# Kernel optimization log

Hardware: AMD Instinct MI355X
Metric: run time of the kernel (lower is better)

The kernel has to match this reference:

```python
import jax, jax.numpy as jnp
import numpy as np

K = 20
NEG_SLOPE = 0.2
BN_EPS = 1e-5


def knn_idx(x, k):
    # x: (B, C, N) -> neighbor indices (B, N, k) by largest negative sq-distance
    xt = jnp.swapaxes(x, 1, 2)                      # (B, N, C)
    inner = 2.0 * jnp.einsum('bic,bjc->bij', xt, xt)
    sq = jnp.sum(xt * xt, axis=-1)                  # (B, N)
    dist = inner - sq[:, :, None] - sq[:, None, :]  # -||xi-xj||^2
    _, idx = jax.lax.top_k(dist, k)
    return idx


def edge_feature(x, src, idx):
    # x: (B, C, N) centers; src: (B, C, M) gather source; idx: (B, N, k)
    xt = jnp.swapaxes(x, 1, 2)                      # (B, N, C)
    st = jnp.swapaxes(src, 1, 2)                    # (B, M, C)
    b = jnp.arange(xt.shape[0])[:, None, None]
    neigh = st[b, idx]                              # (B, N, k, C)
    center = xt[:, :, None, :]                      # (B, N, 1, C)
    feat = jnp.concatenate(
        [neigh - center, jnp.broadcast_to(center, neigh.shape)], axis=-1)
    return jnp.transpose(feat, (0, 3, 1, 2))        # (B, 2C, N, k)


def conv_bn_lrelu(x, w, gamma, beta):
    # 1x1 conv (no bias) + training-mode BatchNorm2d + LeakyReLU(0.2)
    y = jnp.einsum('oc,bcnk->bonk', w, x)
    mean = jnp.mean(y, axis=(0, 2, 3), keepdims=True)
    var = jnp.var(y, axis=(0, 2, 3), keepdims=True)
    y = (y - mean) * jax.lax.rsqrt(var + BN_EPS)
    y = y * gamma[None, :, None, None] + beta[None, :, None, None]
    return jnp.where(y >= 0, y, NEG_SLOPE * y)


def knn_ia_idx(x, y, k):
    # cosine-similarity KNN from x (B,Cx,N) into y (B,Cy,M), normalize over channels
    xn = x / jnp.maximum(jnp.linalg.norm(x, axis=1, keepdims=True), 1e-12)
    yn = y / jnp.maximum(jnp.linalg.norm(y, axis=1, keepdims=True), 1e-12)
    simi = jnp.einsum('bci,bcj->bij', xn, yn)       # (B, N, M)
    _, idx = jax.lax.top_k(simi, k)
    return idx


def setup_inputs() -> dict:
    key = jax.random.key(0)
    ks = jax.random.split(key, 8)
    B, N, M, EMB = 8, 1024, 1024, 512
    x = jax.random.normal(ks[0], (B, 3, N), dtype=jnp.float32)
    y = jax.random.normal(ks[1], (B, 128, M), dtype=jnp.float32)
    def w(k_, o, c):
        return jax.random.normal(k_, (o, c), dtype=jnp.float32) * (1.0 / np.sqrt(c))
    inp = {
        'x': x, 'y': y,
        'w1': w(ks[2], 64, 6),
        'w2': w(ks[3], 64, 128),
        'w3': w(ks[4], 128, 128),
        'w4': w(ks[5], 256, 256),
        'w5': w(ks[6], EMB, 512),
        'g1': jnp.ones(64), 'b1': jnp.zeros(64),
        'g2': jnp.ones(64), 'b2': jnp.zeros(64),
        'g3': jnp.ones(128), 'b3': jnp.zeros(128),
        'g4': jnp.ones(256), 'b4': jnp.zeros(256),
        'g5': jnp.ones(EMB), 'b5': jnp.zeros(EMB),
    }
    return inp


def reference(x, y, w1, w2, w3, w4, w5, g1, b1, g2, b2, g3, b3, g4, b4, g5, b5):
    # block 1
    h = conv_bn_lrelu(edge_feature(x, x, knn_idx(x, K)), w1, g1, b1)
    x1 = jnp.max(h, axis=-1)                        # (B, 64, N)
    # block 2
    h = conv_bn_lrelu(edge_feature(x1, x1, knn_idx(x1, K)), w2, g2, b2)
    x2 = jnp.max(h, axis=-1)                        # (B, 64, N)
    # block 3
    h = conv_bn_lrelu(edge_feature(x2, x2, knn_idx(x2, K)), w3, g3, b3)
    x3 = jnp.max(h, axis=-1)                        # (B, 128, N)
    # block 4: cross-attention KNN into y (cosine similarity)
    h = conv_bn_lrelu(edge_feature(x3, y, knn_ia_idx(x3, y, K)), w4, g4, b4)
    x4 = jnp.max(h, axis=-1)                        # (B, 256, N)
    # final 1x1 conv + BN + LeakyReLU on concatenated features (512 ch)
    cat = jnp.concatenate([x1, x2, x3, x4], axis=1)  # (B, 512, N)
    out = conv_bn_lrelu(cat[..., None], w5, g5, b5)[..., 0]
    return out                                       # (B, n_emb_dims, N)
```

## Files before the change

kernel.cpp:

```cpp
#include <hip/hip_runtime.h>
#include <hip/hip_bf16.h>

#define KNN 20
#define NEG_SLOPE 0.2f

constexpr int BB = 8;
constexpr int NN = 1024;
constexpr int MM = 1024;

typedef short bf16x8 __attribute__((ext_vector_type(8)));
typedef float f32x4 __attribute__((ext_vector_type(4)));
typedef double f64x4 __attribute__((ext_vector_type(4)));
typedef unsigned long long u64;

__device__ __forceinline__ u64 pack_key64(double d, int j) {
  u64 u = (u64)__double_as_longlong(d);
  u = (u & 0x8000000000000000ULL) ? ~u : (u | 0x8000000000000000ULL);
  return (u & ~(u64)1023) | (u64)(1023 - j);
}

__device__ __forceinline__ void topk20_u64(u64 (&s)[16], int lane, int* op) {
#pragma unroll
  for (int p = 1; p < 16; p <<= 1) {
#pragma unroll
    for (int k = p; k >= 1; k >>= 1) {
#pragma unroll
      for (int j = k % p; j + k < 16; j += 2 * k) {
#pragma unroll
        for (int i = 0; i < k; ++i) {
          int a = j + i, b = j + i + k;
          if (b < 16 && (a / (2 * p)) == (b / (2 * p))) {
            u64 hi = s[a] > s[b] ? s[a] : s[b];
            u64 lo = s[a] > s[b] ? s[b] : s[a];
            s[a] = hi;
            s[b] = lo;
          }
        }
      }
    }
  }
#pragma unroll
  for (int r = 0; r < KNN; ++r) {
    u64 win = s[0];
#pragma unroll
    for (int off = 32; off > 0; off >>= 1) {
      u64 o = __shfl_xor(win, off, 64);
      win = o > win ? o : win;
    }
    if (lane == 0) op[r] = 1023 - (int)(win & (u64)1023);
    if (s[0] == win) {
#pragma unroll
      for (int i = 0; i < 15; ++i) s[i] = s[i + 1];
      s[15] = 0ULL;
    }
  }
}

__global__ void k_probe_mfma(int* __restrict__ rowt, int* __restrict__ colt,
                             int* __restrict__ flag) {
  __shared__ int cnt[256];
  __shared__ int oksh;
  int tid = threadIdx.x;
  if (tid == 0) oksh = 1;
  for (int e = tid; e < 256; e += 64) cnt[e] = 0;
  __syncthreads();
  int lane = tid & 63;
  f64x4 z = {0.0, 0.0, 0.0, 0.0};
  double ai = (double)(lane & 15);
  double p3 = 1.0, p5 = 1.0;
  int kq = lane >> 4;
  for (int t = 0; t < kq; ++t) { p3 *= 3.0; p5 *= 5.0; }
  f64x4 d1 = __builtin_amdgcn_mfma_f64_16x16x4f64(ai, 1.0, z, 0, 0, 0);
  f64x4 d2 = __builtin_amdgcn_mfma_f64_16x16x4f64(1.0, ai, z, 0, 0, 0);
  f64x4 d3 = __builtin_amdgcn_mfma_f64_16x16x4f64(p3, p5, z, 0, 0, 0);
  bool ok = true;
  int ri[4], ci[4];
#pragma unroll
  for (int r = 0; r < 4; ++r) {
    double va = d1[r], vb = d2[r], vp = d3[r];
    int i = (int)(va * 0.25);
    int j = (int)(vb * 0.25);
    bool e_ok = (i >= 0) && (i < 16) && (j >= 0) && (j < 16) &&
                (va == 4.0 * (double)i) && (vb == 4.0 * (double)j) && (vp == 3616.0);
    if (e_ok) {
      atomicAdd(&cnt[i * 16 + j], 1);
    } else {
      ok = false;
      i = 0;
      j = 0;
    }
    ri[r] = i;
    ci[r] = j;
  }
  if (!ok) atomicExch(&oksh, 0);
  __syncthreads();
  bool bij = true;
  for (int e = tid; e < 256; e += 64)
    if (cnt[e] != 1) bij = false;
  if (!bij) atomicExch(&oksh, 0);
  __syncthreads();
#pragma unroll
  for (int r = 0; r < 4; ++r) {
    rowt[lane * 4 + r] = ri[r];
    colt[lane * 4 + r] = ci[r];
  }
  if (tid == 0) *flag = oksh;
}

__global__ __launch_bounds__(256) void k_transpose_d(
    const float* __restrict__ in, double* __restrict__ out, int C, int Np) {
  int total = BB * C * Np;
  for (int t = blockIdx.x * 256 + threadIdx.x; t < total; t += gridDim.x * 256) {
    int c = t % C;
    int n = (t / C) % Np;
    int b = t / (C * Np);
    out[t] = (double)in[((size_t)b * C + c) * Np + n];
  }
}

__global__ __launch_bounds__(256) void k_cvt_bf16(
    const float* __restrict__ in, __hip_bfloat16* __restrict__ out, int n) {
  int i = blockIdx.x * 256 + threadIdx.x;
  if (i < n) out[i] = __float2bfloat16(in[i]);
}

template <int RECIP>
__global__ __launch_bounds__(256) void k_rowsq(
    const double* __restrict__ A, int ld, int C, double* __restrict__ sq) {
  int p = blockIdx.x * 256 + threadIdx.x;
  if (p >= BB * NN) return;
  const double* row = A + (size_t)p * ld;
  double s = 0.0;
  for (int c = 0; c < C; ++c) { double v = row[c]; s += v * v; }
  if (RECIP) {
    sq[p] = 1.0 / fmax(sqrt(s), 1e-12);
  } else {
    sq[p] = s;
  }
}

__global__ __launch_bounds__(256) void k_knn3(
    const double* __restrict__ xs3, const double* __restrict__ sq, int* __restrict__ idx) {
  __shared__ double P[NN * 3];
  int b = blockIdx.x;
  const double* Xb = xs3 + (size_t)b * NN * 3;
  int tid = threadIdx.x;
  for (int t = tid; t < NN * 3; t += 256) P[t] = Xb[t];
  __syncthreads();
  int wave = tid >> 6, lane = tid & 63;
  int i = blockIdx.y * 4 + wave;
  double xi = P[i * 3], yi = P[i * 3 + 1], zi = P[i * 3 + 2];
  double sqi = sq[b * NN + i];
  u64 s[16];
#pragma unroll
  for (int m = 0; m < 16; ++m) {
    int j = m * 64 + lane;
    double d = fma(xi, P[j * 3], 0.0);
    d = fma(yi, P[j * 3 + 1], d);
    d = fma(zi, P[j * 3 + 2], d);
    s[m] = pack_key64(2.0 * d - sqi - sq[b * NN + j], j);
  }
  int* op = idx + ((size_t)b * NN + i) * KNN;
  topk20_u64(s, lane, op);
}

template <int MODE>
__global__ __launch_bounds__(256) void k_gram_u(
    const double* __restrict__ A, int lda, const double* __restrict__ Bm, int ldb,
    const double* __restrict__ sqA, const double* __restrict__ sqB,
    u64* __restrict__ kk, int C, int b0, const int* __restrict__ rowt,
    const int* __restrict__ colt, const int* __restrict__ flag) {
  __shared__ double As[2][16][132];
  __shared__ double Bs[2][16][68];
  int bg = b0 + blockIdx.x;
  int bl = blockIdx.x;
  int j0 = blockIdx.y * 64;
  int i0 = blockIdx.z * 128;
  const double* Ab = A + (size_t)bg * NN * lda;
  const double* Bb = Bm + (size_t)bg * MM * ldb;
  int tid = threadIdx.x;
  if (*flag) {
    int lane = tid & 63, w = tid >> 6;
    int lm = lane & 15, lq = lane >> 4;
    f64x4 acc[2][4] = {};
    for (int r = 0; r < 8; ++r) {
      int li = tid + r * 256;
      int row = li >> 4, k = li & 15;
      As[0][k][row] = Ab[(size_t)(i0 + row) * lda + k];
    }
    for (int r = 0; r < 4; ++r) {
      int li = tid + r * 256;
      int row = li >> 4, k = li & 15;
      Bs[0][k][row] = Bb[(size_t)(j0 + row) * ldb + k];
    }
    __syncthreads();
    int nblk = C >> 4;
    for (int cb = 0; cb < nblk; ++cb) {
      int buf = cb & 1;
      double ra[8], rb[4];
      bool pf = (cb + 1 < nblk);
      if (pf) {
        int c0 = (cb + 1) << 4;
        for (int r = 0; r < 8; ++r) {
          int li = tid + r * 256;
          int row = li >> 4, k = li & 15;
          ra[r] = Ab[(size_t)(i0 + row) * lda + c0 + k];
        }
        for (int r = 0; r < 4; ++r) {
          int li = tid + r * 256;
          int row = li >> 4, k = li & 15;
          rb[r] = Bb[(size_t)(j0 + row) * ldb + c0 + k];
        }
      }
#pragma unroll
      for (int kc = 0; kc < 4; ++kc) {
        double a0 = As[buf][kc * 4 + lq][w * 16 + lm];
        double a1 = As[buf][kc * 4 + lq][64 + w * 16 + lm];
#pragma unroll
        for (int t = 0; t < 4; ++t) {
          double b = Bs[buf][kc * 4 + lq][t * 16 + lm];
          acc[0][t] = __builtin_amdgcn_mfma_f64_16x16x4f64(a0, b, acc[0][t], 0, 0, 0);
          acc[1][t] = __builtin_amdgcn_mfma_f64_16x16x4f64(a1, b, acc[1][t], 0, 0, 0);
        }
      }
      if (pf) {
        int nb = buf ^ 1;
        for (int r = 0; r < 8; ++r) {
          int li = tid + r * 256;
          int row = li >> 4, k = li & 15;
          As[nb][k][row] = ra[r];
        }
        for (int r = 0; r < 4; ++r) {
          int li = tid + r * 256;
          int row = li >> 4, k = li & 15;
          Bs[nb][k][row] = rb[r];
        }
      }
      __syncthreads();
    }
    int rta[4], cta[4];
#pragma unroll
    for (int r = 0; r < 4; ++r) {
      rta[r] = rowt[lane * 4 + r];
      cta[r] = colt[lane * 4 + r];
    }
#pragma unroll
    for (int g = 0; g < 2; ++g) {
#pragma unroll
      for (int t = 0; t < 4; ++t) {
#pragma unroll
        for (int r = 0; r < 4; ++r) {
          int i = i0 + g * 64 + w * 16 + rta[r];
          int j = j0 + t * 16 + cta[r];
          double v = acc[g][t][r];
          if (MODE == 1)
            v = 2.0 * v - sqA[(size_t)bg * NN + i] - sqB[(size_t)bg * MM + j];
          if (MODE == 2) v = v * sqA[(size_t)bg * NN + i] * sqB[(size_t)bg * MM + j];
          kk[((size_t)bl * NN + i) * MM + j] = pack_key64(v, j);
        }
      }
    }
  } else {
    int tx = tid & 15, ty = tid >> 4;
    double acc[8][4] = {};
    for (int c0 = 0; c0 < C; c0 += 16) {
      if (c0) __syncthreads();
      for (int r = 0; r < 8; ++r) {
        int li = tid + r * 256;
        int row = li >> 4, k = li & 15;
        As[0][k][row] = Ab[(size_t)(i0 + row) * lda + c0 + k];
      }
      for (int r = 0; r < 4; ++r) {
        int li = tid + r * 256;
        int row = li >> 4, k = li & 15;
        Bs[0][k][row] = Bb[(size_t)(j0 + row) * ldb + c0 + k];
      }
      __syncthreads();
#pragma unroll
      for (int k = 0; k < 16; ++k) {
        double a_[8], b_[4];
#pragma unroll
        for (int ii = 0; ii < 8; ++ii) a_[ii] = As[0][k][ty * 8 + ii];
#pragma unroll
        for (int jj = 0; jj < 4; ++jj) b_[jj] = Bs[0][k][jj * 16 + tx];
#pragma unroll
        for (int ii = 0; ii < 8; ++ii)
#pragma unroll
          for (int jj = 0; jj < 4; ++jj)
            acc[ii][jj] = fma(a_[ii], b_[jj], acc[ii][jj]);
      }
    }
    for (int ii = 0; ii < 8; ++ii) {
      int i = i0 + ty * 8 + ii;
      double qa = sqA[(size_t)bg * NN + i];
      for (int jj = 0; jj < 4; ++jj) {
        int j = j0 + jj * 16 + tx;
        double v = acc[ii][jj];
        if (MODE == 1) v = 2.0 * v - qa - sqB[(size_t)bg * MM + j];
        if (MODE == 2) v = v * qa * sqB[(size_t)bg * MM + j];
        kk[((size_t)bl * NN + i) * MM + j] = pack_key64(v, j);
      }
    }
  }
}

__global__ __launch_bounds__(256) void k_topk(const u64* __restrict__ kk,
                                              int* __restrict__ idx, int b0) {
  int wave = threadIdx.x >> 6;
  int lane = threadIdx.x & 63;
  int bl = blockIdx.x;
  int row = blockIdx.y * 4 + wave;
  const u64* rp = kk + ((size_t)bl * NN + row) * MM;
  u64 s[16];
#pragma unroll
  for (int m = 0; m < 16; ++m) s[m] = rp[m * 64 + lane];
  int* op = idx + ((size_t)(b0 + bl) * NN + row) * KNN;
  topk20_u64(s, lane, op);
}

__global__ __launch_bounds__(256) void k_featmm2(
    const double* __restrict__ src0, int ld0, int Np0,
    const double* __restrict__ src1, int ld1,
    const float* __restrict__ w, int CW,
    double* __restrict__ out0, double* __restrict__ out1, int C, int O,
    const int* __restrict__ rowt, const int* __restrict__ colt,
    const int* __restrict__ flag) {
  __shared__ double As[16][68];
  __shared__ double Ws[16][68];
  int nbo = O >> 6;
  int b = blockIdx.x;
  int mode = blockIdx.y >= nbo;
  int o0 = (blockIdx.y - (mode ? nbo : 0)) * 64;
  int j0 = blockIdx.z * 64;
  const double* src = mode ? src1 : src0;
  int lds_ = mode ? ld1 : ld0;
  int Np = mode ? NN : Np0;
  double* out = mode ? out1 : out0;
  int tid = threadIdx.x;
  const double* Sb = src + (size_t)b * Np * lds_;
  if (*flag) {
    int lane = tid & 63, wv = tid >> 6;
    int lm = lane & 15, lq = lane >> 4;
    f64x4 acc[4] = {};
    for (int c0 = 0; c0 < C; c0 += 16) {
      if (c0) __syncthreads();
      for (int r = 0; r < 4; ++r) {
        int li = tid + r * 256;
        int row = li >> 4, k = li & 15;
        int c = c0 + k;
        As[k][row] = (c < C) ? Sb[(size_t)(j0 + row) * lds_ + c] : 0.0;
        double wvv = 0.0;
        if (c < C) {
          const float* wr = w + (size_t)(o0 + row) * CW;
          wvv = (mode == 0) ? (double)wr[c] : ((double)wr[C + c] - (double)wr[c]);
        }
        Ws[k][row] = wvv;
      }
      __syncthreads();
#pragma unroll
      for (int kc = 0; kc < 4; ++kc) {
        double a = As[kc * 4 + lq][wv * 16 + lm];
#pragma unroll
        for (int t = 0; t < 4; ++t) {
          double bb = Ws[kc * 4 + lq][t * 16 + lm];
          acc[t] = __builtin_amdgcn_mfma_f64_16x16x4f64(a, bb, acc[t], 0, 0, 0);
        }
      }
    }
    int rta[4], cta[4];
#pragma unroll
    for (int r = 0; r < 4; ++r) {
      rta[r] = rowt[lane * 4 + r];
      cta[r] = colt[lane * 4 + r];
    }
#pragma unroll
    for (int t = 0; t < 4; ++t) {
#pragma unroll
      for (int r = 0; r < 4; ++r) {
        int j = j0 + wv * 16 + rta[r];
        int o = o0 + t * 16 + cta[r];
        out[((size_t)b * Np + j) * O + o] = acc[t][r];
      }
    }
  } else {
    int tx = tid & 15, ty = tid >> 4;
    double acc[4][4] = {};
    for (int c0 = 0; c0 < C; c0 += 16) {
      if (c0) __syncthreads();
      for (int r = 0; r < 4; ++r) {
        int li = tid + r * 256;
        int row = li >> 4, k = li & 15;
        int c = c0 + k;
        As[k][row] = (c < C) ? Sb[(size_t)(j0 + row) * lds_ + c] : 0.0;
        double wvv = 0.0;
        if (c < C) {
          const float* wr = w + (size_t)(o0 + row) * CW;
          wvv = (mode == 0) ? (double)wr[c] : ((double)wr[C + c] - (double)wr[c]);
        }
        Ws[k][row] = wvv;
      }
      __syncthreads();
#pragma unroll
      for (int k = 0; k < 16; ++k) {
        double a_[4], b_[4];
#pragma unroll
        for (int ii = 0; ii < 4; ++ii) a_[ii] = As[k][ty * 4 + ii];
#pragma unroll
        for (int jj = 0; jj < 4; ++jj) b_[jj] = Ws[k][tx * 4 + jj];
#pragma unroll
        for (int ii = 0; ii < 4; ++ii)
#pragma unroll
          for (int jj = 0; jj < 4; ++jj)
            acc[ii][jj] = fma(a_[ii], b_[jj], acc[ii][jj]);
      }
    }
    for (int ii = 0; ii < 4; ++ii) {
      int j = j0 + ty * 4 + ii;
      double* op = &out[((size_t)b * Np + j) * O + o0 + tx * 4];
      double2 v0, v1;
      v0.x = acc[ii][0];
      v0.y = acc[ii][1];
      v1.x = acc[ii][2];
      v1.y = acc[ii][3];
      *(double2*)op = v0;
      *(double2*)(op + 2) = v1;
    }
  }
}

__global__ __launch_bounds__(256) void k_gemm5_mfma(
    const __hip_bfloat16* __restrict__ cath, const __hip_bfloat16* __restrict__ w5h,
    float* __restrict__ out) {
  int b = blockIdx.x;
  int j0 = blockIdx.y * 16;
  int o0 = blockIdx.z * 64 + (threadIdx.x >> 6) * 16;
  int lane = threadIdx.x & 63;
  int m = lane & 15;
  int quad = lane >> 4;
  const __hip_bfloat16* arow = cath + ((size_t)b * NN + j0 + m) * 512 + quad * 8;
  const __hip_bfloat16* brow = w5h + (size_t)(o0 + m) * 512 + quad * 8;
  f32x4 acc = {0.f, 0.f, 0.f, 0.f};
#pragma unroll
  for (int c0 = 0; c0 < 512; c0 += 32) {
    bf16x8 a = *(const bf16x8*)(arow + c0);
    bf16x8 bb = *(const bf16x8*)(brow + c0);
    acc = __builtin_amdgcn_mfma_f32_16x16x32_bf16(a, bb, acc, 0, 0, 0);
  }
  float* obase = &out[((size_t)b * NN + j0 + quad * 4) * 512 + o0 + m];
#pragma unroll
  for (int r = 0; r < 4; ++r) obase[(size_t)r * 512] = acc[r];
}

__global__ __launch_bounds__(256) void k_gather(
    const double* __restrict__ u, const double* __restrict__ t, const int* __restrict__ idx,
    double* __restrict__ stats, double* __restrict__ mx, int O, int srcNp) {
  __shared__ int lidx[16 * KNN];
  __shared__ double rs[256];
  __shared__ double rq[256];
  int b = blockIdx.x;
  int n0 = blockIdx.y * 16;
  int o0 = blockIdx.z * 64;
  int tid = threadIdx.x;
  int lane = tid & 63, nsl = tid >> 6;
  for (int w = tid; w < 16 * KNN; w += 256)
    lidx[w] = idx[((size_t)b * NN + n0) * KNN + w];
  __syncthreads();
  int oo = o0 + lane;
  double s1 = 0.0, s2 = 0.0;
  for (int ns = nsl; ns < 16; ns += 4) {
    size_t row = (size_t)b * NN + n0 + ns;
    double tv = t[row * O + oo];
    double mxv = -INFINITY;
    double a1 = 0.0, a2 = 0.0;
#pragma unroll
    for (int k = 0; k < KNN; ++k) {
      int j = lidx[ns * KNN + k];
      double yv = u[((size_t)b * srcNp + j) * O + oo] + tv;
      mxv = fmax(mxv, yv);
      a1 += yv;
      a2 = fma(yv, yv, a2);
    }
    mx[row * O + oo] = mxv;
    s1 += a1;
    s2 += a2;
  }
  rs[tid] = s1;
  rq[tid] = s2;
  __syncthreads();
  if (tid < 64) {
    s1 = rs[tid] + rs[tid + 64] + rs[tid + 128] + rs[tid + 192];
    s2 = rq[tid] + rq[tid + 64] + rq[tid + 128] + rq[tid + 192];
    atomicAdd(&stats[o0 + tid], s1);
    atomicAdd(&stats[O + o0 + tid], s2);
  }
}

__global__ void k_bnfin(const double* __restrict__ stats, const float* __restrict__ gamma,
                        const float* __restrict__ beta, double* __restrict__ sc,
                        int O, double cnt) {
  int o = threadIdx.x;
  if (o >= O) return;
  double mean = stats[o] / cnt;
  double var = stats[O + o] / cnt - mean * mean;
  if (var < 0.0) var = 0.0;
  double rstd = 1.0 / sqrt(var + 1e-5);
  double s = (double)gamma[o] * rstd;
  double c = (double)beta[o] - mean * s;
  sc[o] = s;
  sc[O + o] = c;
}

__global__ __launch_bounds__(256) void k_bnapply(
    const double* __restrict__ mx, const double* __restrict__ u, const double* __restrict__ t,
    const int* __restrict__ idx, const double* __restrict__ sc, double* __restrict__ catd,
    __hip_bfloat16* __restrict__ cath, int coff, int O, int srcNp) {
  int i = blockIdx.x * 256 + threadIdx.x;
  int total = BB * NN * O;
  if (i >= total) return;
  int oo = i % O;
  int n = (i / O) % NN;
  int b = i / (O * NN);
  double s = sc[oo], c = sc[O + oo];
  double v;
  if (s >= 0.0) {
    v = mx[i];
  } else {
    double tv = t[i];
    double mn = INFINITY;
    for (int k = 0; k < KNN; ++k) {
      int j = idx[((size_t)b * NN + n) * KNN + k];
      mn = fmin(mn, u[((size_t)b * srcNp + j) * O + oo] + tv);
    }
    v = mn;
  }
  double a = s * v + c;
  a = (a >= 0.0) ? a : 0.2 * a;
  size_t ci = ((size_t)b * NN + n) * 512 + coff + oo;
  cath[ci] = __float2bfloat16((float)a);
  if (coff < 256) catd[((size_t)b * NN + n) * 256 + coff + oo] = a;
}

__global__ __launch_bounds__(256) void k_stats512(
    const float* __restrict__ y5, double* __restrict__ stats) {
  int b = blockIdx.y;
  int n0 = blockIdx.x * 32;
  int tid = threadIdx.x;
  for (int part = 0; part < 2; ++part) {
    int oo = tid + part * 256;
    float a1 = 0.f, a2 = 0.f;
    for (int ns = 0; ns < 32; ++ns) {
      float v = y5[((size_t)b * NN + n0 + ns) * 512 + oo];
      a1 += v;
      a2 = fmaf(v, v, a2);
    }
    atomicAdd(&stats[oo], (double)a1);
    atomicAdd(&stats[512 + oo], (double)a2);
  }
}

__global__ __launch_bounds__(256) void k_final5b(
    const float* __restrict__ y5, const double* __restrict__ sc, float* __restrict__ out) {
  __shared__ float tile[64][65];
  int b = blockIdx.z;
  int n0 = blockIdx.x * 64;
  int o0 = blockIdx.y * 64;
  int tid = threadIdx.x;
  for (int r = 0; r < 16; ++r) {
    int li = tid + r * 256;
    int nl = li >> 6, ol = li & 63;
    float v = y5[((size_t)b * NN + n0 + nl) * 512 + o0 + ol];
    float a = (float)(sc[o0 + ol] * (double)v + sc[512 + o0 + ol]);
    a = (a >= 0.f) ? a : NEG_SLOPE * a;
    tile[nl][ol] = a;
  }
  __syncthreads();
  for (int r = 0; r < 16; ++r) {
    int li = tid + r * 256;
    int ol = li >> 6, nl = li & 63;
    out[((size_t)b * 512 + o0 + ol) * NN + n0 + nl] = tile[nl][ol];
  }
}

extern "C" void kernel_launch(void* const* d_in, const int* in_sizes, int n_in,
                              void* d_out, int out_size, void* d_ws, size_t ws_size,
                              hipStream_t stream) {
  const float* x = (const float*)d_in[0];
  const float* y = (const float*)d_in[1];
  const float* w1 = (const float*)d_in[2];
  const float* w2 = (const float*)d_in[3];
  const float* w3 = (const float*)d_in[4];
  const float* w4 = (const float*)d_in[5];
  const float* w5 = (const float*)d_in[6];
  const float* g1 = (const float*)d_in[7];
  const float* b1 = (const float*)d_in[8];
  const float* g2 = (const float*)d_in[9];
  const float* b2 = (const float*)d_in[10];
  const float* g3 = (const float*)d_in[11];
  const float* b3 = (const float*)d_in[12];
  const float* g4 = (const float*)d_in[13];
  const float* b4 = (const float*)d_in[14];
  const float* g5 = (const float*)d_in[15];
  const float* b5 = (const float*)d_in[16];

  char* base = (char*)d_ws;
  size_t off = 0;
  auto alloc = [&](size_t bytes) -> char* {
    char* p = base + off;
    off += (bytes + 255) & ~(size_t)255;
    return p;
  };
  double* st = (double*)alloc(1024 * 8);
  double* sc = (double*)alloc(1024 * 8);
  double* sq = (double*)alloc((size_t)BB * NN * 8);
  double* rnx = (double*)alloc((size_t)BB * NN * 8);
  double* rny = (double*)alloc((size_t)BB * MM * 8);
  int* idxb = (int*)alloc((size_t)BB * NN * KNN * 4);
  int* rowt = (int*)alloc(256 * 4);
  int* colt = (int*)alloc(256 * 4);
  int* pflag = (int*)alloc(256);
  double* xs3d = (double*)alloc((size_t)BB * NN * 3 * 8);
  double* ysd = (double*)alloc((size_t)BB * MM * 128 * 8);
  double* catd = (double*)alloc((size_t)BB * NN * 256 * 8);
  __hip_bfloat16* cath = (__hip_bfloat16*)alloc((size_t)BB * NN * 512 * 2);
  __hip_bfloat16* w5h = (__hip_bfloat16*)alloc((size_t)512 * 512 * 2);
  double* uu = (double*)alloc((size_t)BB * MM * 256 * 8);
  double* tt = (double*)alloc((size_t)BB * NN * 256 * 8);
  size_t kkBatchBytes = (size_t)NN * MM * 8;
  size_t avail = (ws_size > off) ? (ws_size - off) : 0;
  int CB = (int)(avail / kkBatchBytes);
  if (CB < 1) CB = 1;
  if (CB > BB) CB = BB;
  u64* KK = (u64*)alloc((size_t)CB * kkBatchBytes);
  float* y5 = (float*)uu;
  double* mx = (double*)d_out;
  float* outp = (float*)d_out;

  const double cntE = (double)BB * NN * KNN;

  auto knn = [&](const double* A, int lda, const double* Bm, int ldb,
                 const double* sa, const double* sb, int C, int mode) {
    for (int b0 = 0; b0 < BB; b0 += CB) {
      int cb = (BB - b0 < CB) ? (BB - b0) : CB;
      dim3 g(cb, MM / 64, NN / 128);
      if (mode == 1)
        k_gram_u<1><<<g, 256, 0, stream>>>(A, lda, Bm, ldb, sa, sb, KK, C, b0, rowt,
                                           colt, pflag);
      else
        k_gram_u<2><<<g, 256, 0, stream>>>(A, lda, Bm, ldb, sa, sb, KK, C, b0, rowt,
                                           colt, pflag);
      k_topk<<<dim3(cb, 256), 256, 0, stream>>>(KK, idxb, b0);
    }
  };

  auto edge_layer = [&](const double* ctr, int ldc, const double* src, int ldsrc,
                        int srcNp, const float* w, int CW, const float* g,
                        const float* bb, int C, int O, int coff) {
    k_featmm2<<<dim3(8, 2 * (O / 64), 16), 256, 0, stream>>>(
        src, ldsrc, srcNp, ctr, ldc, w, CW, uu, tt, C, O, rowt, colt, pflag);
    hipMemsetAsync(st, 0, 1024 * 8, stream);
    k_gather<<<dim3(BB, NN / 16, O / 64), 256, 0, stream>>>(uu, tt, idxb, st, mx, O,
                                                            srcNp);
    k_bnfin<<<1, O, 0, stream>>>(st, g, bb, sc, O, cntE);
    k_bnapply<<<(BB * NN * O + 255) / 256, 256, 0, stream>>>(mx, uu, tt, idxb, sc, catd,
                                                             cath, coff, O, srcNp);
  };

  k_probe_mfma<<<1, 64, 0, stream>>>(rowt, colt, pflag);
  k_transpose_d<<<96, 256, 0, stream>>>(x, xs3d, 3, NN);
  k_transpose_d<<<2048, 256, 0, stream>>>(y, ysd, 128, MM);
  k_cvt_bf16<<<1024, 256, 0, stream>>>(w5, w5h, 512 * 512);

  k_rowsq<0><<<32, 256, 0, stream>>>(xs3d, 3, 3, sq);
  k_knn3<<<dim3(BB, 256), 256, 0, stream>>>(xs3d, sq, idxb);
  edge_layer(xs3d, 3, xs3d, 3, NN, w1, 6, g1, b1, 3, 64, 0);

  k_rowsq<0><<<32, 256, 0, stream>>>(catd, 256, 64, sq);
  knn(catd, 256, catd, 256, sq, sq, 64, 1);
  edge_layer(catd, 256, catd, 256, NN, w2, 128, g2, b2, 64, 64, 64);

  k_rowsq<0><<<32, 256, 0, stream>>>(catd + 64, 256, 64, sq);
  knn(catd + 64, 256, catd + 64, 256, sq, sq, 64, 1);
  edge_layer(catd + 64, 256, catd + 64, 256, NN, w3, 128, g3, b3, 64, 128, 128);

  k_rowsq<1><<<32, 256, 0, stream>>>(catd + 128, 256, 128, rnx);
  k_rowsq<1><<<32, 256, 0, stream>>>(ysd, 128, 128, rny);
  knn(catd + 128, 256, ysd, 128, rnx, rny, 128, 2);
  edge_layer(catd + 128, 256, ysd, 128, MM, w4, 256, g4, b4, 128, 256, 256);

  hipMemsetAsync(st, 0, 1024 * 8, stream);
  k_gemm5_mfma<<<dim3(BB, 64, 8), 256, 0, stream>>>(cath, w5h, y5);
  k_stats512<<<dim3(32, 8), 256, 0, stream>>>(y5, st);
  k_bnfin<<<1, 512, 0, stream>>>(st, g5, b5, sc, 512, (double)(BB * NN));
  k_final5b<<<dim3(16, 8, 8), 256, 0, stream>>>(y5, sc, outp);
}
```

Baseline: 708.7 us.

## Retile gram kernel to single-wave 64x64 blocks and fold BN finalize into consumers

The gram/KNN distance kernel now runs one 64-thread wave per 64x64 output tile, holding a 4x4 grid of MFMA accumulators per wave instead of four waves sharing a double-buffered 128x64 tile. The register prefetch is dropped and the grid doubles along the row dimension. Separately, the BatchNorm finalize kernel is removed: each k_bnapply and k_final5b block recomputes the scale and shift from the stats into shared memory, saving five tiny launches. In exchange, per-wave A/B reuse rises but latency hiding drops without double buffering, and the BN finalize math is repeated in every block.

```diff
diff --git a/kernel.cpp b/kernel.cpp
--- a/kernel.cpp
+++ b/kernel.cpp
@@ -165,78 +165,48 @@
 }
 
 template <int MODE>
-__global__ __launch_bounds__(256) void k_gram_u(
+__global__ __launch_bounds__(64, 2) void k_gram_u(
     const double* __restrict__ A, int lda, const double* __restrict__ Bm, int ldb,
     const double* __restrict__ sqA, const double* __restrict__ sqB,
     u64* __restrict__ kk, int C, int b0, const int* __restrict__ rowt,
     const int* __restrict__ colt, const int* __restrict__ flag) {
-  __shared__ double As[2][16][132];
-  __shared__ double Bs[2][16][68];
+  __shared__ double As[16][69];
+  __shared__ double Bs[16][69];
   int bg = b0 + blockIdx.x;
   int bl = blockIdx.x;
   int j0 = blockIdx.y * 64;
-  int i0 = blockIdx.z * 128;
+  int i0 = blockIdx.z * 64;
   const double* Ab = A + (size_t)bg * NN * lda;
   const double* Bb = Bm + (size_t)bg * MM * ldb;
-  int tid = threadIdx.x;
+  int lane = threadIdx.x;
   if (*flag) {
-    int lane = tid & 63, w = tid >> 6;
     int lm = lane & 15, lq = lane >> 4;
-    f64x4 acc[2][4] = {};
-    for (int r = 0; r < 8; ++r) {
-      int li = tid + r * 256;
-      int row = li >> 4, k = li & 15;
-      As[0][k][row] = Ab[(size_t)(i0 + row) * lda + k];
-    }
-    for (int r = 0; r < 4; ++r) {
-      int li = tid + r * 256;
-      int row = li >> 4, k = li & 15;
-      Bs[0][k][row] = Bb[(size_t)(j0 + row) * ldb + k];
-    }
-    __syncthreads();
-    int nblk = C >> 4;
-    for (int cb = 0; cb < nblk; ++cb) {
-      int buf = cb & 1;
-      double ra[8], rb[4];
-      bool pf = (cb + 1 < nblk);
-      if (pf) {
-        int c0 = (cb + 1) << 4;
-        for (int r = 0; r < 8; ++r) {
-          int li = tid + r * 256;
-          int row = li >> 4, k = li & 15;
-          ra[r] = Ab[(size_t)(i0 + row) * lda + c0 + k];
+    f64x4 acc[4][4] = {};
+    for (int c0 = 0; c0 < C; c0 += 16) {
+      if (c0) __syncthreads();
+#pragma unroll 4
+      for (int r = 0; r < 16; ++r) {
+        int li = lane + r * 64;
+        int row = li >> 4, k = li & 15;
+        As[k][row] = Ab[(size_t)(i0 + row) * lda + c0 + k];
+        Bs[k][row] = Bb[(size_t)(j0 + row) * ldb + c0 + k];
+      }
+      __syncthreads();
+#pragma unroll
+      for (int kc = 0; kc < 4; ++kc) {
+        double a_[4], b_[4];
+#pragma unroll
+        for (int s = 0; s < 4; ++s) {
+          a_[s] = As[kc * 4 + lq][s * 16 + lm];
+          b_[s] = Bs[kc * 4 + lq][s * 16 + lm];
         }
-        for (int r = 0; r < 4; ++r) {
-          int li = tid + r * 256;
-          int row = li >> 4, k = li & 15;
-          rb[r] = Bb[(size_t)(j0 + row) * ldb + c0 + k];
-        }
-      }
-#pragma unroll
-      for (int kc = 0; kc < 4; ++kc) {
-        double a0 = As[buf][kc * 4 + lq][w * 16 + lm];
-        double a1 = As[buf][kc * 4 + lq][64 + w * 16 + lm];
-#pragma unroll
-        for (int t = 0; t < 4; ++t) {
-          double b = Bs[buf][kc * 4 + lq][t * 16 + lm];
-          acc[0][t] = __builtin_amdgcn_mfma_f64_16x16x4f64(a0, b, acc[0][t], 0, 0, 0);
-          acc[1][t] = __builtin_amdgcn_mfma_f64_16x16x4f64(a1, b, acc[1][t], 0, 0, 0);
-        }
-      }
-      if (pf) {
-        int nb = buf ^ 1;
-        for (int r = 0; r < 8; ++r) {
-          int li = tid + r * 256;
-          int row = li >> 4, k = li & 15;
-          As[nb][k][row] = ra[r];
-        }
-        for (int r = 0; r < 4; ++r) {
-          int li = tid + r * 256;
-          int row = li >> 4, k = li & 15;
-          Bs[nb][k][row] = rb[r];
-        }
-      }
-      __syncthreads();
+#pragma unroll
+        for (int si = 0; si < 4; ++si)
+#pragma unroll
+          for (int sj = 0; sj < 4; ++sj)
+            acc[si][sj] =
+                __builtin_amdgcn_mfma_f64_16x16x4f64(a_[si], b_[sj], acc[si][sj], 0, 0, 0);
+      }
     }
     int rta[4], cta[4];
 #pragma unroll
@@ -245,14 +215,14 @@
       cta[r] = colt[lane * 4 + r];
     }
 #pragma unroll
-    for (int g = 0; g < 2; ++g) {
-#pragma unroll
-      for (int t = 0; t < 4; ++t) {
+    for (int si = 0; si < 4; ++si) {
+#pragma unroll
+      for (int sj = 0; sj < 4; ++sj) {
 #pragma unroll
         for (int r = 0; r < 4; ++r) {
-          int i = i0 + g * 64 + w * 16 + rta[r];
-          int j = j0 + t * 16 + cta[r];
-          double v = acc[g][t][r];
+          int i = i0 + si * 16 + rta[r];
+          int j = j0 + sj * 16 + cta[r];
+          double v = acc[si][sj][r];
           if (MODE == 1)
             v = 2.0 * v - sqA[(size_t)bg * NN + i] - sqB[(size_t)bg * MM + j];
           if (MODE == 2) v = v * sqA[(size_t)bg * NN + i] * sqB[(size_t)bg * MM + j];
@@ -261,41 +231,38 @@
       }
     }
   } else {
-    int tx = tid & 15, ty = tid >> 4;
-    double acc[8][4] = {};
+    int lr = lane >> 3, lc = lane & 7;
+    double acc2[8][8] = {};
     for (int c0 = 0; c0 < C; c0 += 16) {
       if (c0) __syncthreads();
-      for (int r = 0; r < 8; ++r) {
-        int li = tid + r * 256;
+      for (int r = 0; r < 16; ++r) {
+        int li = lane + r * 64;
         int row = li >> 4, k = li & 15;
-        As[0][k][row] = Ab[(size_t)(i0 + row) * lda + c0 + k];
-      }
-      for (int r = 0; r < 4; ++r) {
-        int li = tid + r * 256;
-        int row = li >> 4, k = li & 15;
-        Bs[0][k][row] = Bb[(size_t)(j0 + row) * ldb + c0 + k];
+        As[k][row] = Ab[(size_t)(i0 + row) * lda + c0 + k];
+        Bs[k][row] = Bb[(size_t)(j0 + row) * ldb + c0 + k];
       }
       __syncthreads();
 #pragma unroll
       for (int k = 0; k < 16; ++k) {
-        double a_[8], b_[4];
-#pragma unroll
-        for (int ii = 0; ii < 8; ++ii) a_[ii] = As[0][k][ty * 8 + ii];
-#pragma unroll
-        for (int jj = 0; jj < 4; ++jj) b_[jj] = Bs[0][k][jj * 16 + tx];
+        double a_[8], b_[8];
+#pragma unroll
+        for (int t = 0; t < 8; ++t) {
+          a_[t] = As[k][lr * 8 + t];
+          b_[t] = Bs[k][lc * 8 + t];
+        }
 #pragma unroll
         for (int ii = 0; ii < 8; ++ii)
 #pragma unroll
-          for (int jj = 0; jj < 4; ++jj)
-            acc[ii][jj] = fma(a_[ii], b_[jj], acc[ii][jj]);
+          for (int jj = 0; jj < 8; ++jj)
+            acc2[ii][jj] = fma(a_[ii], b_[jj], acc2[ii][jj]);
       }
     }
     for (int ii = 0; ii < 8; ++ii) {
-      int i = i0 + ty * 8 + ii;
+      int i = i0 + lr * 8 + ii;
       double qa = sqA[(size_t)bg * NN + i];
-      for (int jj = 0; jj < 4; ++jj) {
-        int j = j0 + jj * 16 + tx;
-        double v = acc[ii][jj];
+      for (int jj = 0; jj < 8; ++jj) {
+        int j = j0 + lc * 8 + jj;
+        double v = acc2[ii][jj];
         if (MODE == 1) v = 2.0 * v - qa - sqB[(size_t)bg * MM + j];
         if (MODE == 2) v = v * qa * sqB[(size_t)bg * MM + j];
         kk[((size_t)bl * NN + i) * MM + j] = pack_key64(v, j);
@@ -495,32 +462,32 @@
   }
 }
 
-__global__ void k_bnfin(const double* __restrict__ stats, const float* __restrict__ gamma,
-                        const float* __restrict__ beta, double* __restrict__ sc,
-                        int O, double cnt) {
-  int o = threadIdx.x;
-  if (o >= O) return;
-  double mean = stats[o] / cnt;
-  double var = stats[O + o] / cnt - mean * mean;
-  if (var < 0.0) var = 0.0;
-  double rstd = 1.0 / sqrt(var + 1e-5);
-  double s = (double)gamma[o] * rstd;
-  double c = (double)beta[o] - mean * s;
-  sc[o] = s;
-  sc[O + o] = c;
-}
-
 __global__ __launch_bounds__(256) void k_bnapply(
     const double* __restrict__ mx, const double* __restrict__ u, const double* __restrict__ t,
-    const int* __restrict__ idx, const double* __restrict__ sc, double* __restrict__ catd,
-    __hip_bfloat16* __restrict__ cath, int coff, int O, int srcNp) {
-  int i = blockIdx.x * 256 + threadIdx.x;
+    const int* __restrict__ idx, const double* __restrict__ stats,
+    const float* __restrict__ gamma, const float* __restrict__ beta, double cnt,
+    double* __restrict__ catd, __hip_bfloat16* __restrict__ cath, int coff, int O,
+    int srcNp) {
+  __shared__ double scs[256];
+  __shared__ double scc[256];
+  int tid = threadIdx.x;
+  if (tid < O) {
+    double mean = stats[tid] / cnt;
+    double var = stats[O + tid] / cnt - mean * mean;
+    if (var < 0.0) var = 0.0;
+    double rstd = 1.0 / sqrt(var + 1e-5);
+    double s = (double)gamma[tid] * rstd;
+    scs[tid] = s;
+    scc[tid] = (double)beta[tid] - mean * s;
+  }
+  __syncthreads();
+  int i = blockIdx.x * 256 + tid;
   int total = BB * NN * O;
   if (i >= total) return;
   int oo = i % O;
   int n = (i / O) % NN;
   int b = i / (O * NN);
-  double s = sc[oo], c = sc[O + oo];
+  double s = scs[oo], c = scc[oo];
   double v;
   if (s >= 0.0) {
     v = mx[i];
@@ -559,17 +526,33 @@
 }
 
 __global__ __launch_bounds__(256) void k_final5b(
-    const float* __restrict__ y5, const double* __restrict__ sc, float* __restrict__ out) {
+    const float* __restrict__ y5, const double* __restrict__ stats,
+    const float* __restrict__ g5, const float* __restrict__ b5,
+    float* __restrict__ out) {
   __shared__ float tile[64][65];
+  __shared__ double scs[64];
+  __shared__ double scc[64];
   int b = blockIdx.z;
   int n0 = blockIdx.x * 64;
   int o0 = blockIdx.y * 64;
   int tid = threadIdx.x;
+  if (tid < 64) {
+    int o = o0 + tid;
+    double cnt = (double)(BB * NN);
+    double mean = stats[o] / cnt;
+    double var = stats[512 + o] / cnt - mean * mean;
+    if (var < 0.0) var = 0.0;
+    double rstd = 1.0 / sqrt(var + 1e-5);
+    double s = (double)g5[o] * rstd;
+    scs[tid] = s;
+    scc[tid] = (double)b5[o] - mean * s;
+  }
+  __syncthreads();
   for (int r = 0; r < 16; ++r) {
     int li = tid + r * 256;
     int nl = li >> 6, ol = li & 63;
     float v = y5[((size_t)b * NN + n0 + nl) * 512 + o0 + ol];
-    float a = (float)(sc[o0 + ol] * (double)v + sc[512 + o0 + ol]);
+    float a = (float)(scs[ol] * (double)v + scc[ol]);
     a = (a >= 0.f) ? a : NEG_SLOPE * a;
     tile[nl][ol] = a;
   }
@@ -610,7 +593,6 @@
     return p;
   };
   double* st = (double*)alloc(1024 * 8);
-  double* sc = (double*)alloc(1024 * 8);
   double* sq = (double*)alloc((size_t)BB * NN * 8);
   double* rnx = (double*)alloc((size_t)BB * NN * 8);
   double* rny = (double*)alloc((size_t)BB * MM * 8);
@@ -641,13 +623,13 @@
                  const double* sa, const double* sb, int C, int mode) {
     for (int b0 = 0; b0 < BB; b0 += CB) {
       int cb = (BB - b0 < CB) ? (BB - b0) : CB;
-      dim3 g(cb, MM / 64, NN / 128);
+      dim3 g(cb, MM / 64, NN / 64);
       if (mode == 1)
-        k_gram_u<1><<<g, 256, 0, stream>>>(A, lda, Bm, ldb, sa, sb, KK, C, b0, rowt,
-                                           colt, pflag);
+        k_gram_u<1><<<g, 64, 0, stream>>>(A, lda, Bm, ldb, sa, sb, KK, C, b0, rowt,
+                                          colt, pflag);
       else
-        k_gram_u<2><<<g, 256, 0, stream>>>(A, lda, Bm, ldb, sa, sb, KK, C, b0, rowt,
-                                           colt, pflag);
+        k_gram_u<2><<<g, 64, 0, stream>>>(A, lda, Bm, ldb, sa, sb, KK, C, b0, rowt,
+                                          colt, pflag);
       k_topk<<<dim3(cb, 256), 256, 0, stream>>>(KK, idxb, b0);
     }
   };
@@ -660,9 +642,8 @@
     hipMemsetAsync(st, 0, 1024 * 8, stream);
     k_gather<<<dim3(BB, NN / 16, O / 64), 256, 0, stream>>>(uu, tt, idxb, st, mx, O,
                                                             srcNp);
-    k_bnfin<<<1, O, 0, stream>>>(st, g, bb, sc, O, cntE);
-    k_bnapply<<<(BB * NN * O + 255) / 256, 256, 0, stream>>>(mx, uu, tt, idxb, sc, catd,
-                                                             cath, coff, O, srcNp);
+    k_bnapply<<<(BB * NN * O + 255) / 256, 256, 0, stream>>>(
+        mx, uu, tt, idxb, st, g, bb, cntE, catd, cath, coff, O, srcNp);
   };
 
   k_probe_mfma<<<1, 64, 0, stream>>>(rowt, colt, pflag);
@@ -690,6 +671,5 @@
   hipMemsetAsync(st, 0, 1024 * 8, stream);
   k_gemm5_mfma<<<dim3(BB, 64, 8), 256, 0, stream>>>(cath, w5h, y5);
   k_stats512<<<dim3(32, 8), 256, 0, stream>>>(y5, st);
-  k_bnfin<<<1, 512, 0, stream>>>(st, g5, b5, sc, 512, (double)(BB * NN));
-  k_final5b<<<dim3(16, 8, 8), 256, 0, stream>>>(y5, sc, outp);
-}
+  k_final5b<<<dim3(16, 8, 8), 256, 0, stream>>>(y5, st, g5, b5, outp);
+}
```

Measured after the change: 709.0 us. About the same (+0.0%).
